# Performance work log

Hardware: AMD Instinct MI355X
Metric: run time of the kernel (lower is better)

## Reference

```python
import jax, jax.numpy as jnp
import numpy as np

C = 64
K = 16
DEPTH = 4            # int(sqrt(K))
N_NODES = K - 1      # 15 internal nodes per subspace tree
D = 512              # input feature dim, D // C = 8 per subspace
M = 512              # output dim (LUT rows)
N = 16384            # number of input rows


def _make_selection_matrix(C, depth=DEPTH):
    # row i within a subspace selects the transformed dim used at tree level of node i
    lvl = [0, 1, 1, 2, 2, 2, 2, 3, 3, 3, 3, 3, 3, 3, 3]
    S = np.zeros((C * N_NODES, C * depth), np.float32)
    for c in range(C):
        for i in range(N_NODES):
            S[c * N_NODES + i, c * depth + lvl[i]] = 1.0
    return S


def _make_bit_matrix(C, K=K):
    # per-subspace (K, K-1) matrix: leaf k gets +/-1 on the 4 nodes along its root-to-leaf path
    Bm = np.zeros((K, N_NODES), np.float32)
    for k in range(K):
        node = 0
        for l in range(DEPTH):
            bit = (k >> (DEPTH - 1 - l)) & 1
            Bm[k, node] = 1.0 if bit else -1.0
            node = 2 * node + 1 + bit  # children of node i are 2i+1 (left) and 2i+2 (right)
    Bfull = np.zeros((C * K, C * N_NODES), np.float32)
    for c in range(C):
        Bfull[c * K:(c + 1) * K, c * N_NODES:(c + 1) * N_NODES] = Bm
    return Bfull


def setup_inputs() -> dict:
    key = jax.random.key(0)
    k1, k2, k3, k4 = jax.random.split(key, 4)
    I = jax.random.normal(k1, (N, D), dtype=jnp.float32)
    A = jax.random.normal(k2, (C, D // C, DEPTH), dtype=jnp.float32) * (1.0 / np.sqrt(D // C))
    T = jax.random.normal(k3, (C * N_NODES,), dtype=jnp.float32) * 0.1
    L = jax.random.normal(k4, (M, C, K), dtype=jnp.float32)
    S = jnp.asarray(_make_selection_matrix(C))
    B = jnp.asarray(_make_bit_matrix(C))
    return {"I": I, "A": A, "T": T, "L": L, "S": S, "B": B}


def reference(I, A, T, L, S, B):
    C_, sub, depth = A.shape
    Kq = L.shape[-1]
    n = I.shape[0]
    # block-diagonal per-subspace projection: (n, D) -> (n, C*depth)
    Ir = I.T.reshape(C_, sub, n)                      # (C, sub, n)
    xt = jnp.einsum('csn,csd->cdn', Ir, A)            # (C, depth, n)
    xt = xt.reshape(C_ * depth, n)                    # (C*depth, n)
    # tree encoding: per-node activations, tanh relaxation, leaf scores
    h = S @ xt - T[:, None]                           # (C*15, n)
    b = (B @ jnp.tanh(h)).reshape(C_, Kq, n)          # (C, K, n)
    # straight-through hard one-hot encoding with softmax backward
    E_soft = jax.nn.softmax(b, axis=1)
    E_hard = jax.nn.one_hot(jnp.argmax(b, axis=1), Kq, axis=1, dtype=b.dtype)
    E = E_hard + E_soft - jax.lax.stop_gradient(E_soft)  # (C, K, n)
    # LUT decode: out[n, m] = sum_c L[m, c, enc(n, c)]
    out = jnp.einsum('mck,ckn->nm', L, E)
    return out
```

## Files before the change

### kernel.cpp

```cpp
#include <hip/hip_runtime.h>
#include <hip/hip_fp16.h>
#include <math.h>

#define CC 64
#define KK 16
#define NNODES 15
#define DD 512
#define MM 512
#define NN 16384
#define KG 1024

#define BM 128
#define BJ 128
#define BK 32
#define LDA 40

typedef _Float16 half8_t __attribute__((ext_vector_type(8)));
typedef float float4_t __attribute__((ext_vector_type(4)));

__device__ __forceinline__ float xla_tanhf(float x) {
    const float kMax = 7.90531110763549805f;
    bool tiny = fabsf(x) < 0.0004f;
    float xc = fminf(fmaxf(x, -kMax), kMax);
    float x2 = __fmul_rn(xc, xc);
    float p = __fmaf_rn(x2, -2.76076847742355e-16f, 2.00018790482477e-13f);
    p = __fmaf_rn(x2, p, -8.60467152213735e-11f);
    p = __fmaf_rn(x2, p, 5.12229709037114e-08f);
    p = __fmaf_rn(x2, p, 1.48572235717979e-05f);
    p = __fmaf_rn(x2, p, 6.37261928875436e-04f);
    p = __fmaf_rn(x2, p, 4.89352455891786e-03f);
    p = __fmul_rn(xc, p);
    float q = __fmaf_rn(x2, 1.19825839466702e-06f, 1.18534705686654e-04f);
    q = __fmaf_rn(x2, q, 2.26843463243900e-03f);
    q = __fmaf_rn(x2, q, 4.89352518554385e-03f);
    return tiny ? x : __fdiv_rn(p, q);
}

__global__ __launch_bounds__(256) void convert_lut(const float* __restrict__ L,
                                                   __half* __restrict__ Lh) {
    int gid = blockIdx.x * 256 + threadIdx.x;
    float4 v = ((const float4*)L)[gid];
    __half2 a = __floats2half2_rn(v.x, v.y);
    __half2 b = __floats2half2_rn(v.z, v.w);
    ((__half2*)Lh)[2 * gid]     = a;
    ((__half2*)Lh)[2 * gid + 1] = b;
}

__global__ __launch_bounds__(256) void encode_kernel(const float* __restrict__ I,
                                                     const float* __restrict__ A,
                                                     const float* __restrict__ T,
                                                     unsigned char* __restrict__ idx) {
    __shared__ float sAT[32 * 64];
    __shared__ float sTT[NNODES * 64];
    const int tid = threadIdx.x;
    for (int g = tid; g < 32 * 64; g += 256)
        sAT[g] = A[((g & 63) << 5) + (g >> 6)];
    for (int g = tid; g < NNODES * 64; g += 256)
        sTT[g] = T[(g & 63) * NNODES + (g >> 6)];
    __syncthreads();

    int gid = blockIdx.x * 256 + tid;
    int j = gid >> 6;
    int c = gid & 63;

    const float* Ij = I + (size_t)j * DD + c * 8;
    float4 v0 = ((const float4*)Ij)[0];
    float4 v1 = ((const float4*)Ij)[1];
    float iv[8] = {v0.x, v0.y, v0.z, v0.w, v1.x, v1.y, v1.z, v1.w};

    float t[4] = {0.f, 0.f, 0.f, 0.f};
#pragma unroll
    for (int s = 0; s < 8; ++s) {
        float v = iv[s];
#pragma unroll
        for (int d = 0; d < 4; ++d)
            t[d] = __fmaf_rn(v, sAT[(s * 4 + d) * 64 + c], t[d]);
    }

    const int lvl[NNODES] = {0, 1, 1, 2, 2, 2, 2, 3, 3, 3, 3, 3, 3, 3, 3};
    float th[NNODES];
#pragma unroll
    for (int i = 0; i < NNODES; ++i) {
        float h = __fsub_rn(t[lvl[i]], sTT[i * 64 + c]);
        th[i] = xla_tanhf(h);
    }

    int best = 0;
    float bestv = -3.0e38f;
#pragma unroll
    for (int k = 0; k < KK; ++k) {
        int node = 0;
        float s = 0.f;
#pragma unroll
        for (int l = 0; l < 4; ++l) {
            int bit = (k >> (3 - l)) & 1;
            s = __fadd_rn(s, bit ? th[node] : -th[node]);
            node = 2 * node + 1 + bit;
        }
        if (s > bestv) { bestv = s; best = k; }
    }
    idx[gid] = (unsigned char)best;
}

__global__ __launch_bounds__(256, 2) void gemm_decode(const __half* __restrict__ Lh,
                                                      const unsigned char* __restrict__ idx,
                                                      float* __restrict__ out) {
    __shared__ __half sA[2][BM * LDA];
    __shared__ unsigned char sCode[CC * BJ];

    const int tid = threadIdx.x;
    const int m0 = (blockIdx.x & 3) * BM;
    const int j0 = (blockIdx.x >> 2) * BJ;

    {
        const unsigned int* g = (const unsigned int*)(idx + (size_t)j0 * CC);
#pragma unroll
        for (int it = 0; it < 8; ++it) {
            int wi = it * 256 + tid;
            unsigned int wv = g[wi];
            int jl = (wi * 4) >> 6;
            int c  = (wi * 4) & 63;
            sCode[(c + 0) * BJ + jl] = (unsigned char)(wv & 0xff);
            sCode[(c + 1) * BJ + jl] = (unsigned char)((wv >> 8) & 0xff);
            sCode[(c + 2) * BJ + jl] = (unsigned char)((wv >> 16) & 0xff);
            sCode[(c + 3) * BJ + jl] = (unsigned char)(wv >> 24);
        }
    }

    const int sr   = tid >> 1;
    const int sseg = tid & 1;
    {
        const __half* gs = Lh + (size_t)(m0 + sr) * KG + sseg * 16;
        uint4 va = *(const uint4*)(gs);
        uint4 vb = *(const uint4*)(gs + 8);
        __half* ld = (__half*)sA[0] + sr * LDA + sseg * 16;
        *(uint4*)ld = va;
        *(uint4*)(ld + 8) = vb;
    }
    __syncthreads();

    const int lane = tid & 63;
    const int wv2  = tid >> 6;
    const int jw   = (wv2 & 1) * 64;
    const int mw   = (wv2 >> 1) * 64;
    const int l15  = lane & 15;
    const int quad = lane >> 4;
    const int kpar8 = (quad & 1) * 8;
    const int chalf = quad >> 1;

    float4_t acc[4][4];
#pragma unroll
    for (int rf = 0; rf < 4; ++rf)
#pragma unroll
        for (int cf = 0; cf < 4; ++cf) acc[rf][cf] = (float4_t){0.f, 0.f, 0.f, 0.f};

    int buf = 0;
    for (int step = 0; step < 32; ++step) {
        uint4 pva, pvb;
        if (step < 31) {
            const __half* gs = Lh + (size_t)(m0 + sr) * KG + (step + 1) * BK + sseg * 16;
            pva = *(const uint4*)(gs);
            pvb = *(const uint4*)(gs + 8);
        }

        half8_t a[4];
#pragma unroll
        for (int rf = 0; rf < 4; ++rf)
            a[rf] = *(const half8_t*)((const __half*)sA[buf] + (mw + rf * 16 + l15) * LDA + quad * 8);

        const int cbase = step * 2 + chalf;
        half8_t b[4];
#pragma unroll
        for (int cf = 0; cf < 4; ++cf) {
            int code = sCode[cbase * BJ + jw + cf * 16 + l15];
            int p = code - kpar8;
            int h = p >> 1;
            unsigned int sel = (p & 1) ? 0x3C000000u : 0x00003C00u;
            uint4 bw;
            bw.x = (h == 0) ? sel : 0u;
            bw.y = (h == 1) ? sel : 0u;
            bw.z = (h == 2) ? sel : 0u;
            bw.w = (h == 3) ? sel : 0u;
            b[cf] = *(half8_t*)&bw;
        }

#pragma unroll
        for (int rf = 0; rf < 4; ++rf)
#pragma unroll
            for (int cf = 0; cf < 4; ++cf)
                acc[rf][cf] = __builtin_amdgcn_mfma_f32_16x16x32_f16(a[rf], b[cf], acc[rf][cf], 0, 0, 0);

        __syncthreads();
        if (step < 31) {
            __half* ld = (__half*)sA[buf ^ 1] + sr * LDA + sseg * 16;
            *(uint4*)ld = pva;
            *(uint4*)(ld + 8) = pvb;
            buf ^= 1;
        }
        __syncthreads();
    }

#pragma unroll
    for (int rf = 0; rf < 4; ++rf)
#pragma unroll
        for (int cf = 0; cf < 4; ++cf) {
            int j = j0 + jw + cf * 16 + l15;
            int m = m0 + mw + rf * 16 + quad * 4;
            *(float4*)(out + (size_t)j * MM + m) =
                make_float4(acc[rf][cf][0], acc[rf][cf][1], acc[rf][cf][2], acc[rf][cf][3]);
        }
}

extern "C" void kernel_launch(void* const* d_in, const int* in_sizes, int n_in,
                              void* d_out, int out_size, void* d_ws, size_t ws_size,
                              hipStream_t stream) {
    const float* I = (const float*)d_in[0];
    const float* A = (const float*)d_in[1];
    const float* T = (const float*)d_in[2];
    const float* L = (const float*)d_in[3];

    __half* Lh = (__half*)d_ws;
    unsigned char* idx = (unsigned char*)d_ws + (1 << 20);
    float* out = (float*)d_out;

    hipLaunchKernelGGL(convert_lut, dim3((MM * KG / 4) / 256), dim3(256), 0, stream, L, Lh);
    hipLaunchKernelGGL(encode_kernel, dim3((NN * CC) / 256), dim3(256), 0, stream, I, A, T, idx);
    hipLaunchKernelGGL(gemm_decode, dim3((NN / BJ) * (MM / BM)), dim3(256), 0, stream, Lh, idx, out);
}
```

Measured before the change: 140.8 us.

## Read LUT directly from global in decode GEMM, drop LDS staging and syncs

The decode GEMM no longer stages LUT tiles through double-buffered shared memory with two barriers per step. Each wave now loads its A fragments straight from global/L2, since the half LUT is 1 MB and cache resident. Codes are kept as packed 32-bit words in a padded LDS array, and the tile shrinks to 128x64 with 4 waves each covering 32 rows, targeting 4 blocks per CU. In exchange, each block issues more redundant global loads and has less register reuse per tile.

```diff
diff --git a/kernel.cpp b/kernel.cpp
--- a/kernel.cpp
+++ b/kernel.cpp
@@ -11,9 +11,7 @@
 #define KG 1024
 
 #define BM 128
-#define BJ 128
-#define BK 32
-#define LDA 40
+#define BJ 64
 
 typedef _Float16 half8_t __attribute__((ext_vector_type(8)));
 typedef float float4_t __attribute__((ext_vector_type(4)));
@@ -102,11 +100,10 @@
     idx[gid] = (unsigned char)best;
 }
 
-__global__ __launch_bounds__(256, 2) void gemm_decode(const __half* __restrict__ Lh,
+__global__ __launch_bounds__(256, 4) void gemm_decode(const __half* __restrict__ Lh,
                                                       const unsigned char* __restrict__ idx,
                                                       float* __restrict__ out) {
-    __shared__ __half sA[2][BM * LDA];
-    __shared__ unsigned char sCode[CC * BJ];
+    __shared__ unsigned int sIdxW[BJ * 17];
 
     const int tid = threadIdx.x;
     const int m0 = (blockIdx.x & 3) * BM;
@@ -115,96 +112,74 @@
     {
         const unsigned int* g = (const unsigned int*)(idx + (size_t)j0 * CC);
 #pragma unroll
-        for (int it = 0; it < 8; ++it) {
+        for (int it = 0; it < 4; ++it) {
             int wi = it * 256 + tid;
-            unsigned int wv = g[wi];
-            int jl = (wi * 4) >> 6;
-            int c  = (wi * 4) & 63;
-            sCode[(c + 0) * BJ + jl] = (unsigned char)(wv & 0xff);
-            sCode[(c + 1) * BJ + jl] = (unsigned char)((wv >> 8) & 0xff);
-            sCode[(c + 2) * BJ + jl] = (unsigned char)((wv >> 16) & 0xff);
-            sCode[(c + 3) * BJ + jl] = (unsigned char)(wv >> 24);
-        }
-    }
-
-    const int sr   = tid >> 1;
-    const int sseg = tid & 1;
-    {
-        const __half* gs = Lh + (size_t)(m0 + sr) * KG + sseg * 16;
-        uint4 va = *(const uint4*)(gs);
-        uint4 vb = *(const uint4*)(gs + 8);
-        __half* ld = (__half*)sA[0] + sr * LDA + sseg * 16;
-        *(uint4*)ld = va;
-        *(uint4*)(ld + 8) = vb;
+            int jl = wi >> 4;
+            int s  = wi & 15;
+            sIdxW[jl * 17 + s] = g[wi];
+        }
     }
     __syncthreads();
 
-    const int lane = tid & 63;
-    const int wv2  = tid >> 6;
-    const int jw   = (wv2 & 1) * 64;
-    const int mw   = (wv2 >> 1) * 64;
-    const int l15  = lane & 15;
-    const int quad = lane >> 4;
+    const int lane  = tid & 63;
+    const int wv2   = tid >> 6;
+    const int mw    = wv2 * 32;
+    const int l15   = lane & 15;
+    const int quad  = lane >> 4;
     const int kpar8 = (quad & 1) * 8;
     const int chalf = quad >> 1;
-
-    float4_t acc[4][4];
-#pragma unroll
-    for (int rf = 0; rf < 4; ++rf)
+    const int shft  = 8 * chalf;
+
+    float4_t acc[2][4];
+#pragma unroll
+    for (int rf = 0; rf < 2; ++rf)
 #pragma unroll
         for (int cf = 0; cf < 4; ++cf) acc[rf][cf] = (float4_t){0.f, 0.f, 0.f, 0.f};
 
-    int buf = 0;
-    for (int step = 0; step < 32; ++step) {
-        uint4 pva, pvb;
-        if (step < 31) {
-            const __half* gs = Lh + (size_t)(m0 + sr) * KG + (step + 1) * BK + sseg * 16;
-            pva = *(const uint4*)(gs);
-            pvb = *(const uint4*)(gs + 8);
-        }
-
-        half8_t a[4];
-#pragma unroll
-        for (int rf = 0; rf < 4; ++rf)
-            a[rf] = *(const half8_t*)((const __half*)sA[buf] + (mw + rf * 16 + l15) * LDA + quad * 8);
-
-        const int cbase = step * 2 + chalf;
-        half8_t b[4];
+    const __half* abase = Lh + (size_t)(m0 + mw + l15) * KG + quad * 8;
+
+    for (int sp = 0; sp < 16; ++sp) {
+        unsigned int cw0 = sIdxW[(0 * 16 + l15) * 17 + sp];
+        unsigned int cw1 = sIdxW[(1 * 16 + l15) * 17 + sp];
+        unsigned int cw2 = sIdxW[(2 * 16 + l15) * 17 + sp];
+        unsigned int cw3 = sIdxW[(3 * 16 + l15) * 17 + sp];
+
+#pragma unroll
+        for (int t = 0; t < 2; ++t) {
+            const int step = sp * 2 + t;
+
+            half8_t a0 = *(const half8_t*)(abase + 0 * 16 * KG + step * 32);
+            half8_t a1 = *(const half8_t*)(abase + 1 * 16 * KG + step * 32);
+
+            unsigned int cws[4] = {cw0, cw1, cw2, cw3};
+            half8_t b[4];
+#pragma unroll
+            for (int cf = 0; cf < 4; ++cf) {
+                int code = (int)((cws[cf] >> (shft + 16 * t)) & 0xffu);
+                int p = code - kpar8;
+                int h = p >> 1;
+                unsigned int sel = (p & 1) ? 0x3C000000u : 0x00003C00u;
+                uint4 bw;
+                bw.x = (h == 0) ? sel : 0u;
+                bw.y = (h == 1) ? sel : 0u;
+                bw.z = (h == 2) ? sel : 0u;
+                bw.w = (h == 3) ? sel : 0u;
+                b[cf] = *(half8_t*)&bw;
+            }
+
+#pragma unroll
+            for (int cf = 0; cf < 4; ++cf) {
+                acc[0][cf] = __builtin_amdgcn_mfma_f32_16x16x32_f16(a0, b[cf], acc[0][cf], 0, 0, 0);
+                acc[1][cf] = __builtin_amdgcn_mfma_f32_16x16x32_f16(a1, b[cf], acc[1][cf], 0, 0, 0);
+            }
+        }
+    }
+
+#pragma unroll
+    for (int rf = 0; rf < 2; ++rf)
 #pragma unroll
         for (int cf = 0; cf < 4; ++cf) {
-            int code = sCode[cbase * BJ + jw + cf * 16 + l15];
-            int p = code - kpar8;
-            int h = p >> 1;
-            unsigned int sel = (p & 1) ? 0x3C000000u : 0x00003C00u;
-            uint4 bw;
-            bw.x = (h == 0) ? sel : 0u;
-            bw.y = (h == 1) ? sel : 0u;
-            bw.z = (h == 2) ? sel : 0u;
-            bw.w = (h == 3) ? sel : 0u;
-            b[cf] = *(half8_t*)&bw;
-        }
-
-#pragma unroll
-        for (int rf = 0; rf < 4; ++rf)
-#pragma unroll
-            for (int cf = 0; cf < 4; ++cf)
-                acc[rf][cf] = __builtin_amdgcn_mfma_f32_16x16x32_f16(a[rf], b[cf], acc[rf][cf], 0, 0, 0);
-
-        __syncthreads();
-        if (step < 31) {
-            __half* ld = (__half*)sA[buf ^ 1] + sr * LDA + sseg * 16;
-            *(uint4*)ld = pva;
-            *(uint4*)(ld + 8) = pvb;
-            buf ^= 1;
-        }
-        __syncthreads();
-    }
-
-#pragma unroll
-    for (int rf = 0; rf < 4; ++rf)
-#pragma unroll
-        for (int cf = 0; cf < 4; ++cf) {
-            int j = j0 + jw + cf * 16 + l15;
+            int j = j0 + cf * 16 + l15;
             int m = m0 + mw + rf * 16 + quad * 4;
             *(float4*)(out + (size_t)j * MM + m) =
                 make_float4(acc[rf][cf][0], acc[rf][cf][1], acc[rf][cf][2], acc[rf][cf][3]);
@@ -225,5 +200,5 @@
 
     hipLaunchKernelGGL(convert_lut, dim3((MM * KG / 4) / 256), dim3(256), 0, stream, L, Lh);
     hipLaunchKernelGGL(encode_kernel, dim3((NN * CC) / 256), dim3(256), 0, stream, I, A, T, idx);
-    hipLaunchKernelGGL(gemm_decode, dim3((NN / BJ) * (MM / BM)), dim3(256), 0, stream, Lh, idx, out);
-}
+    hipLaunchKernelGGL(gemm_decode, dim3((MM / BM) * (NN / BJ)), dim3(256), 0, stream, Lh, idx, out);
+}
```

New measurement: 146.9 us. 1.04x slower.
